# Kernel optimization log

Hardware: AMD Instinct MI355X
Metric: run time of the kernel (lower is better)

Reference implementation:

```python
import jax, jax.numpy as jnp
import numpy as np

C = 256

def setup_inputs() -> dict:
    key = jax.random.key(0)
    ks = jax.random.split(key, 9)
    B, H, W = 32, 32, 32
    s = C ** -0.5  # init scale for weights
    inputs = jax.random.normal(ks[0], (B, H, W, C), jnp.float32)
    Wq = jax.random.normal(ks[1], (C, C), jnp.float32) * s
    Wk = jax.random.normal(ks[2], (C, C), jnp.float32) * s
    Wv = jax.random.normal(ks[3], (C, C), jnp.float32) * s
    Wo = jax.random.normal(ks[4], (C, C), jnp.float32) * s
    bq = jnp.zeros((C,), jnp.float32)
    bk = jnp.zeros((C,), jnp.float32)
    bv = jnp.zeros((C,), jnp.float32)
    bo = jnp.zeros((C,), jnp.float32)
    return {"inputs": inputs, "Wq": Wq, "bq": bq, "Wk": Wk, "bk": bk,
            "Wv": Wv, "bv": bv, "Wo": Wo, "bo": bo}

def reference(inputs, Wq, bq, Wk, bk, Wv, bv, Wo, bo):
    B, H, W, c = inputs.shape
    scale = jnp.float32(c) ** -0.5
    x = inputs.reshape(B, H * W, c)           # 1x1 conv == per-pixel matmul
    q = x @ Wq + bq                           # [B, HW, C]
    k = x @ Wk + bk
    v = x @ Wv + bv
    scores = jnp.einsum('bnc,bmc->bnm', q, k) * scale  # [B, HW, HW]
    attn = jax.nn.softmax(scores, axis=-1)
    attended = jnp.einsum('bnm,bmc->bnc', attn, v)     # [B, HW, C]
    out = attended @ Wo + bo
    return out.reshape(B, H, W, c)
```

## Files before the change

kernel.cpp:

```cpp
#include <hip/hip_runtime.h>
#include <hip/hip_bf16.h>

typedef __bf16 bf16;
typedef __bf16 bf16x8 __attribute__((ext_vector_type(8)));
typedef float f32x4 __attribute__((ext_vector_type(4)));

#define SM_C 0.09016994374947424f

__global__ __launch_bounds__(256) void transpose_w(
    const float* __restrict__ Wq, const float* __restrict__ Wk,
    const float* __restrict__ Wv, const float* __restrict__ Wo,
    bf16* __restrict__ Wt)
{
    int idx = blockIdx.x * 256 + threadIdx.x;
    int m = idx >> 16, r = idx & 65535;
    int n = r >> 8, k = r & 255;
    const float* W = (m == 0) ? Wq : (m == 1) ? Wk : (m == 2) ? Wv : Wo;
    Wt[(size_t)m * 65536 + n * 256 + k] = (bf16)W[k * 256 + n];
}

__global__ __launch_bounds__(256) void qkv_gemm(
    const float* __restrict__ X, const bf16* __restrict__ Wt,
    const float* __restrict__ bq, const float* __restrict__ bk,
    const float* __restrict__ bv,
    bf16* __restrict__ Qo, bf16* __restrict__ Ko, bf16* __restrict__ Vto)
{
    __shared__ bf16 Xs[128 * 264];
    __shared__ bf16 Ws[2][64 * 264];

    const int t    = threadIdx.x;
    const int lane = t & 63, wv = t >> 6;
    const int quad = lane >> 4, l16 = lane & 15;
    const int bm   = blockIdx.x;

    const int m0 = t >> 3;
    const int c0 = (t & 7) * 8;

#pragma unroll
    for (int p = 0; p < 4; ++p) {
#pragma unroll
        for (int kt = 0; kt < 4; ++kt) {
            const float* px = X + (size_t)(bm * 128 + m0 + p * 32) * 256 + kt * 64 + c0;
            f32x4 a = *(const f32x4*)px, b = *(const f32x4*)(px + 4);
            bf16x8 r;
#pragma unroll
            for (int j = 0; j < 4; ++j) { r[j] = (bf16)a[j]; r[j + 4] = (bf16)b[j]; }
            *(bf16x8*)(Xs + (m0 + p * 32) * 264 + kt * 64 + c0) = r;
        }
    }

    const int w0 = t >> 2;
    const int wc = (t & 3) * 8;

    bf16x8 wreg[8];
#pragma unroll
    for (int c = 0; c < 8; ++c)
        wreg[c] = *(const bf16x8*)(Wt + (size_t)w0 * 256 + c * 32 + wc);
#pragma unroll
    for (int c = 0; c < 8; ++c)
        *(bf16x8*)(Ws[0] + w0 * 264 + c * 32 + wc) = wreg[c];
#pragma unroll
    for (int c = 0; c < 8; ++c)
        wreg[c] = *(const bf16x8*)(Wt + (size_t)16384 + w0 * 256 + c * 32 + wc);

    for (int o = 0; o < 12; ++o) {
        __syncthreads();

        if (o < 11) {
#pragma unroll
            for (int c = 0; c < 8; ++c)
                *(bf16x8*)(Ws[(o + 1) & 1] + w0 * 264 + c * 32 + wc) = wreg[c];
            if (o < 10) {
#pragma unroll
                for (int c = 0; c < 8; ++c)
                    wreg[c] = *(const bf16x8*)(Wt + (size_t)(o + 2) * 16384 + w0 * 256 + c * 32 + wc);
            }
        }

        const bf16* Wb = Ws[o & 1];
        const f32x4 zero = {0.0f, 0.0f, 0.0f, 0.0f};
        f32x4 acc[2][4];
        for (int i = 0; i < 2; ++i)
            for (int j = 0; j < 4; ++j) acc[i][j] = zero;

#pragma unroll
        for (int ks = 0; ks < 8; ++ks) {
            bf16x8 a[2], bb[4];
#pragma unroll
            for (int mt = 0; mt < 2; ++mt)
                a[mt] = *(const bf16x8*)(Xs + (wv * 32 + mt * 16 + l16) * 264 + ks * 32 + quad * 8);
#pragma unroll
            for (int nt = 0; nt < 4; ++nt)
                bb[nt] = *(const bf16x8*)(Wb + (nt * 16 + l16) * 264 + ks * 32 + quad * 8);
#pragma unroll
            for (int mt = 0; mt < 2; ++mt)
#pragma unroll
                for (int nt = 0; nt < 4; ++nt)
                    acc[mt][nt] = __builtin_amdgcn_mfma_f32_16x16x32_bf16(
                        a[mt], bb[nt], acc[mt][nt], 0, 0, 0);
        }

        const int proj = o >> 2, nt4 = o & 3;
        const float* bias = (proj == 0) ? bq : (proj == 1) ? bk : bv;
#pragma unroll
        for (int nt = 0; nt < 4; ++nt) {
            int col = nt4 * 64 + nt * 16 + l16;
            float bvv = bias[col];
#pragma unroll
            for (int mt = 0; mt < 2; ++mt) {
#pragma unroll
                for (int r = 0; r < 4; ++r) {
                    int grow = bm * 128 + wv * 32 + mt * 16 + quad * 4 + r;
                    float v = acc[mt][nt][r] + bvv;
                    if (proj == 0) {
                        Qo[(size_t)grow * 256 + col] = (bf16)v;
                    } else if (proj == 1) {
                        Ko[(size_t)grow * 256 + col] = (bf16)v;
                    } else {
                        int b = grow >> 10, m = grow & 1023;
                        Vto[(size_t)b * 262144 + (size_t)col * 1024 + m] = (bf16)v;
                    }
                }
            }
        }
    }
}

__global__ __launch_bounds__(256, 1) void flash_attn(
    const bf16* __restrict__ Qr, const bf16* __restrict__ K,
    const bf16* __restrict__ Vt, bf16* __restrict__ A)
{
    __shared__ bf16 Ks[2][32 * 264];
    __shared__ bf16 Vs[2][256 * 40];
    __shared__ bf16 Ps[4][32 * 32];

    const int t    = threadIdx.x;
    const int lane = t & 63, wv = t >> 6;
    const int quad = lane >> 4, l16 = lane & 15;
    const int b  = blockIdx.x;
    const int qt = blockIdx.y;

    bf16x8 qf[2][8];
#pragma unroll
    for (int mt = 0; mt < 2; ++mt) {
        const size_t qrow = (size_t)b * 1024 + qt * 128 + wv * 32 + mt * 16 + l16;
#pragma unroll
        for (int ks = 0; ks < 8; ++ks)
            qf[mt][ks] = *(const bf16x8*)(Qr + qrow * 256 + ks * 32 + quad * 8);
    }

    const f32x4 zero = {0.0f, 0.0f, 0.0f, 0.0f};
    f32x4 o[2][16];
    for (int mt = 0; mt < 2; ++mt)
        for (int n = 0; n < 16; ++n) o[mt][n] = zero;
    float lst[2][4] = {{0.f, 0.f, 0.f, 0.f}, {0.f, 0.f, 0.f, 0.f}};

    char* Pb = (char*)(Ps[wv]);

    const int kv0 = t >> 5, kc0 = (t & 31) * 8;
    const int vc0 = t >> 2, vm0 = (t & 3) * 8;

    bf16x8 kp[4], vp[4];
#pragma unroll
    for (int p = 0; p < 4; ++p) {
        kp[p] = *(const bf16x8*)(K + (size_t)(b * 1024 + kv0 + p * 8) * 256 + kc0);
        vp[p] = *(const bf16x8*)(Vt + (size_t)b * 262144 + (size_t)(vc0 + p * 64) * 1024 + vm0);
    }
#pragma unroll
    for (int p = 0; p < 4; ++p) {
        *(bf16x8*)(Ks[0] + (kv0 + p * 8) * 264 + kc0) = kp[p];
        *(bf16x8*)(Vs[0] + (vc0 + p * 64) * 40 + vm0) = vp[p];
    }
#pragma unroll
    for (int p = 0; p < 4; ++p) {
        kp[p] = *(const bf16x8*)(K + (size_t)(b * 1024 + 32 + kv0 + p * 8) * 256 + kc0);
        vp[p] = *(const bf16x8*)(Vt + (size_t)b * 262144 + (size_t)(vc0 + p * 64) * 1024 + 32 + vm0);
    }

    for (int j = 0; j < 32; ++j) {
        const bf16* Kb = Ks[j & 1];
        const bf16* Vb = Vs[j & 1];
        __syncthreads();

        f32x4 s[2][2];
        s[0][0] = zero; s[0][1] = zero; s[1][0] = zero; s[1][1] = zero;
#pragma unroll
        for (int ks = 0; ks < 8; ++ks) {
#pragma unroll
            for (int n = 0; n < 2; ++n) {
                bf16x8 bfr = *(const bf16x8*)(Kb + (n * 16 + l16) * 264 + ks * 32 + quad * 8);
                s[0][n] = __builtin_amdgcn_mfma_f32_16x16x32_bf16(qf[0][ks], bfr, s[0][n], 0, 0, 0);
                s[1][n] = __builtin_amdgcn_mfma_f32_16x16x32_bf16(qf[1][ks], bfr, s[1][n], 0, 0, 0);
            }
        }

        if (j < 31) {
            bf16* Kn = Ks[(j + 1) & 1];
            bf16* Vn = Vs[(j + 1) & 1];
#pragma unroll
            for (int p = 0; p < 4; ++p) {
                *(bf16x8*)(Kn + (kv0 + p * 8) * 264 + kc0) = kp[p];
                *(bf16x8*)(Vn + (vc0 + p * 64) * 40 + vm0) = vp[p];
            }
            if (j < 30) {
#pragma unroll
                for (int p = 0; p < 4; ++p) {
                    kp[p] = *(const bf16x8*)(K + (size_t)(b * 1024 + (j + 2) * 32 + kv0 + p * 8) * 256 + kc0);
                    vp[p] = *(const bf16x8*)(Vt + (size_t)b * 262144 + (size_t)(vc0 + p * 64) * 1024 + (j + 2) * 32 + vm0);
                }
            }
        }

#pragma unroll
        for (int mt = 0; mt < 2; ++mt) {
#pragma unroll
            for (int n = 0; n < 2; ++n) {
#pragma unroll
                for (int r = 0; r < 4; ++r) {
                    float pv = __builtin_amdgcn_exp2f(s[mt][n][r] * SM_C);
                    lst[mt][r] += pv;
                    int row = mt * 16 + quad * 4 + r;
                    *(bf16*)(Pb + ((row * 64 + n * 32 + l16 * 2) ^ ((row & 7) << 4))) = (bf16)pv;
                }
            }
        }

        bf16x8 af0 = *(const bf16x8*)(Pb + ((l16 * 64 + quad * 16) ^ ((l16 & 7) << 4)));
        bf16x8 af1 = *(const bf16x8*)(Pb + (((16 + l16) * 64 + quad * 16) ^ ((l16 & 7) << 4)));
#pragma unroll
        for (int n = 0; n < 16; ++n) {
            bf16x8 bfr = *(const bf16x8*)(Vb + (n * 16 + l16) * 40 + quad * 8);
            o[0][n] = __builtin_amdgcn_mfma_f32_16x16x32_bf16(af0, bfr, o[0][n], 0, 0, 0);
            o[1][n] = __builtin_amdgcn_mfma_f32_16x16x32_bf16(af1, bfr, o[1][n], 0, 0, 0);
        }
    }

#pragma unroll
    for (int mt = 0; mt < 2; ++mt) {
#pragma unroll
        for (int r = 0; r < 4; ++r) {
            float l = lst[mt][r];
            for (int off = 1; off < 16; off <<= 1)
                l += __shfl_xor(l, off, 64);
            float inv = 1.0f / l;
            size_t grow = (size_t)b * 1024 + qt * 128 + wv * 32 + mt * 16 + quad * 4 + r;
#pragma unroll
            for (int n = 0; n < 16; ++n)
                A[grow * 256 + n * 16 + l16] = (bf16)(o[mt][n][r] * inv);
        }
    }
}

__global__ __launch_bounds__(256) void oproj_gemm(
    const bf16* __restrict__ Xv, const bf16* __restrict__ W,
    const float* __restrict__ bias, float* __restrict__ outv)
{
    __shared__ bf16 Xs[128 * 72];
    __shared__ bf16 Ws[64 * 72];

    const int t    = threadIdx.x;
    const int lane = t & 63, wv = t >> 6;
    const int quad = lane >> 4, l16 = lane & 15;
    const int bm = blockIdx.x;
    const int bn = blockIdx.y;

    const f32x4 zero = {0.0f, 0.0f, 0.0f, 0.0f};
    f32x4 acc[2][4];
    for (int i = 0; i < 2; ++i)
        for (int j = 0; j < 4; ++j) acc[i][j] = zero;

    const int m0 = t >> 3;
    const int c0 = (t & 7) * 8;

    bf16x8 xp[4], wp[2];
#pragma unroll
    for (int p = 0; p < 4; ++p)
        xp[p] = *(const bf16x8*)(Xv + (size_t)(bm * 128 + m0 + p * 32) * 256 + c0);
#pragma unroll
    for (int p = 0; p < 2; ++p)
        wp[p] = *(const bf16x8*)(W + (size_t)(bn * 64 + m0 + p * 32) * 256 + c0);

    for (int kt = 0; kt < 4; ++kt) {
#pragma unroll
        for (int p = 0; p < 4; ++p)
            *(bf16x8*)(Xs + (m0 + p * 32) * 72 + c0) = xp[p];
#pragma unroll
        for (int p = 0; p < 2; ++p)
            *(bf16x8*)(Ws + (m0 + p * 32) * 72 + c0) = wp[p];
        __syncthreads();

        if (kt < 3) {
#pragma unroll
            for (int p = 0; p < 4; ++p)
                xp[p] = *(const bf16x8*)(Xv + (size_t)(bm * 128 + m0 + p * 32) * 256 + (kt + 1) * 64 + c0);
#pragma unroll
            for (int p = 0; p < 2; ++p)
                wp[p] = *(const bf16x8*)(W + (size_t)(bn * 64 + m0 + p * 32) * 256 + (kt + 1) * 64 + c0);
        }

#pragma unroll
        for (int ks = 0; ks < 2; ++ks) {
            bf16x8 a[2], bb[4];
            for (int mt = 0; mt < 2; ++mt)
                a[mt] = *(const bf16x8*)(Xs + (wv * 32 + mt * 16 + l16) * 72 + ks * 32 + quad * 8);
            for (int nt = 0; nt < 4; ++nt)
                bb[nt] = *(const bf16x8*)(Ws + (nt * 16 + l16) * 72 + ks * 32 + quad * 8);
            for (int mt = 0; mt < 2; ++mt)
                for (int nt = 0; nt < 4; ++nt)
                    acc[mt][nt] = __builtin_amdgcn_mfma_f32_16x16x32_bf16(
                        a[mt], bb[nt], acc[mt][nt], 0, 0, 0);
        }
        __syncthreads();
    }

#pragma unroll
    for (int nt = 0; nt < 4; ++nt) {
        int col = bn * 64 + nt * 16 + l16;
        float bvv = bias[col];
#pragma unroll
        for (int mt = 0; mt < 2; ++mt)
#pragma unroll
            for (int r = 0; r < 4; ++r) {
                int grow = bm * 128 + wv * 32 + mt * 16 + quad * 4 + r;
                outv[(size_t)grow * 256 + col] = acc[mt][nt][r] + bvv;
            }
    }
}

extern "C" void kernel_launch(void* const* d_in, const int* in_sizes, int n_in,
                              void* d_out, int out_size, void* d_ws, size_t ws_size,
                              hipStream_t stream)
{
    (void)in_sizes; (void)n_in; (void)out_size; (void)ws_size;
    const float* X  = (const float*)d_in[0];
    const float* Wq = (const float*)d_in[1];
    const float* bq = (const float*)d_in[2];
    const float* Wk = (const float*)d_in[3];
    const float* bk = (const float*)d_in[4];
    const float* Wv = (const float*)d_in[5];
    const float* bv = (const float*)d_in[6];
    const float* Wo = (const float*)d_in[7];
    const float* bo = (const float*)d_in[8];
    float* out = (float*)d_out;

    const size_t NTOK = (size_t)32768 * 256;

    bf16* Wt  = (bf16*)d_ws;
    bf16* Qw  = (bf16*)d_ws + 262144;
    bf16* Kw  = Qw + NTOK;
    bf16* Vtw = Kw + NTOK;

    transpose_w<<<1024, 256, 0, stream>>>(Wq, Wk, Wv, Wo, Wt);
    qkv_gemm   <<<256,  256, 0, stream>>>(X, Wt, bq, bk, bv, Qw, Kw, Vtw);
    flash_attn <<<dim3(32, 8),  256, 0, stream>>>(Qw, Kw, Vtw, Qw);
    oproj_gemm <<<dim3(256, 4), 256, 0, stream>>>(Qw, Wt + 3 * 65536, bo, out);
}
```

Baseline: 198.7 us.

## Double waves per block in QKV GEMM and flash attention kernels

Both the QKV projection and flash attention kernels go from 256 to 512 threads per block. Each wave now owns 16 query/token rows instead of 32, and the cooperative load indexing is remapped for 512 threads. The grid stays at 256 blocks, so the aim is more waves per CU to hide latency and better use of the MFMA units, with lower register pressure per wave. The cost is that each wave reuses every shared-memory K/V and weight fragment for half as many rows, so LDS read traffic per FLOP doubles.

```diff
diff --git a/kernel.cpp b/kernel.cpp
--- a/kernel.cpp
+++ b/kernel.cpp
@@ -19,7 +19,7 @@
     Wt[(size_t)m * 65536 + n * 256 + k] = (bf16)W[k * 256 + n];
 }
 
-__global__ __launch_bounds__(256) void qkv_gemm(
+__global__ __launch_bounds__(512, 2) void qkv_gemm(
     const float* __restrict__ X, const bf16* __restrict__ Wt,
     const float* __restrict__ bq, const float* __restrict__ bk,
     const float* __restrict__ bv,
@@ -33,71 +33,66 @@
     const int quad = lane >> 4, l16 = lane & 15;
     const int bm   = blockIdx.x;
 
-    const int m0 = t >> 3;
-    const int c0 = (t & 7) * 8;
-
-#pragma unroll
-    for (int p = 0; p < 4; ++p) {
-#pragma unroll
-        for (int kt = 0; kt < 4; ++kt) {
-            const float* px = X + (size_t)(bm * 128 + m0 + p * 32) * 256 + kt * 64 + c0;
-            f32x4 a = *(const f32x4*)px, b = *(const f32x4*)(px + 4);
-            bf16x8 r;
-#pragma unroll
-            for (int j = 0; j < 4; ++j) { r[j] = (bf16)a[j]; r[j + 4] = (bf16)b[j]; }
-            *(bf16x8*)(Xs + (m0 + p * 32) * 264 + kt * 64 + c0) = r;
-        }
-    }
-
-    const int w0 = t >> 2;
-    const int wc = (t & 3) * 8;
-
-    bf16x8 wreg[8];
-#pragma unroll
-    for (int c = 0; c < 8; ++c)
-        wreg[c] = *(const bf16x8*)(Wt + (size_t)w0 * 256 + c * 32 + wc);
-#pragma unroll
-    for (int c = 0; c < 8; ++c)
-        *(bf16x8*)(Ws[0] + w0 * 264 + c * 32 + wc) = wreg[c];
-#pragma unroll
-    for (int c = 0; c < 8; ++c)
-        wreg[c] = *(const bf16x8*)(Wt + (size_t)16384 + w0 * 256 + c * 32 + wc);
+#pragma unroll
+    for (int i = 0; i < 8; ++i) {
+        int c = t + i * 512;
+        int row = c >> 5, cf = (c & 31) * 8;
+        const float* px = X + (size_t)(bm * 128 + row) * 256 + cf;
+        f32x4 a = *(const f32x4*)px, b = *(const f32x4*)(px + 4);
+        bf16x8 r;
+#pragma unroll
+        for (int j = 0; j < 4; ++j) { r[j] = (bf16)a[j]; r[j + 4] = (bf16)b[j]; }
+        *(bf16x8*)(Xs + row * 264 + cf) = r;
+    }
+
+    bf16x8 wreg[4];
+#pragma unroll
+    for (int i = 0; i < 4; ++i) {
+        int c = t + i * 512;
+        wreg[i] = *(const bf16x8*)(Wt + (size_t)(c >> 5) * 256 + (c & 31) * 8);
+    }
+#pragma unroll
+    for (int i = 0; i < 4; ++i) {
+        int c = t + i * 512;
+        *(bf16x8*)(Ws[0] + (c >> 5) * 264 + (c & 31) * 8) = wreg[i];
+    }
+#pragma unroll
+    for (int i = 0; i < 4; ++i) {
+        int c = t + i * 512;
+        wreg[i] = *(const bf16x8*)(Wt + (size_t)16384 + (c >> 5) * 256 + (c & 31) * 8);
+    }
 
     for (int o = 0; o < 12; ++o) {
         __syncthreads();
 
         if (o < 11) {
 #pragma unroll
-            for (int c = 0; c < 8; ++c)
-                *(bf16x8*)(Ws[(o + 1) & 1] + w0 * 264 + c * 32 + wc) = wreg[c];
+            for (int i = 0; i < 4; ++i) {
+                int c = t + i * 512;
+                *(bf16x8*)(Ws[(o + 1) & 1] + (c >> 5) * 264 + (c & 31) * 8) = wreg[i];
+            }
             if (o < 10) {
 #pragma unroll
-                for (int c = 0; c < 8; ++c)
-                    wreg[c] = *(const bf16x8*)(Wt + (size_t)(o + 2) * 16384 + w0 * 256 + c * 32 + wc);
+                for (int i = 0; i < 4; ++i) {
+                    int c = t + i * 512;
+                    wreg[i] = *(const bf16x8*)(Wt + (size_t)(o + 2) * 16384 + (c >> 5) * 256 + (c & 31) * 8);
+                }
             }
         }
 
         const bf16* Wb = Ws[o & 1];
         const f32x4 zero = {0.0f, 0.0f, 0.0f, 0.0f};
-        f32x4 acc[2][4];
-        for (int i = 0; i < 2; ++i)
-            for (int j = 0; j < 4; ++j) acc[i][j] = zero;
+        f32x4 acc[4];
+        acc[0] = zero; acc[1] = zero; acc[2] = zero; acc[3] = zero;
 
 #pragma unroll
         for (int ks = 0; ks < 8; ++ks) {
-            bf16x8 a[2], bb[4];
-#pragma unroll
-            for (int mt = 0; mt < 2; ++mt)
-                a[mt] = *(const bf16x8*)(Xs + (wv * 32 + mt * 16 + l16) * 264 + ks * 32 + quad * 8);
-#pragma unroll
-            for (int nt = 0; nt < 4; ++nt)
-                bb[nt] = *(const bf16x8*)(Wb + (nt * 16 + l16) * 264 + ks * 32 + quad * 8);
-#pragma unroll
-            for (int mt = 0; mt < 2; ++mt)
-#pragma unroll
-                for (int nt = 0; nt < 4; ++nt)
-                    acc[mt][nt] = __builtin_amdgcn_mfma_f32_16x16x32_bf16(
-                        a[mt], bb[nt], acc[mt][nt], 0, 0, 0);
+            bf16x8 a = *(const bf16x8*)(Xs + (wv * 16 + l16) * 264 + ks * 32 + quad * 8);
+#pragma unroll
+            for (int nt = 0; nt < 4; ++nt) {
+                bf16x8 bb = *(const bf16x8*)(Wb + (nt * 16 + l16) * 264 + ks * 32 + quad * 8);
+                acc[nt] = __builtin_amdgcn_mfma_f32_16x16x32_bf16(a, bb, acc[nt], 0, 0, 0);
+            }
         }
 
         const int proj = o >> 2, nt4 = o & 3;
@@ -107,32 +102,29 @@
             int col = nt4 * 64 + nt * 16 + l16;
             float bvv = bias[col];
 #pragma unroll
-            for (int mt = 0; mt < 2; ++mt) {
-#pragma unroll
-                for (int r = 0; r < 4; ++r) {
-                    int grow = bm * 128 + wv * 32 + mt * 16 + quad * 4 + r;
-                    float v = acc[mt][nt][r] + bvv;
-                    if (proj == 0) {
-                        Qo[(size_t)grow * 256 + col] = (bf16)v;
-                    } else if (proj == 1) {
-                        Ko[(size_t)grow * 256 + col] = (bf16)v;
-                    } else {
-                        int b = grow >> 10, m = grow & 1023;
-                        Vto[(size_t)b * 262144 + (size_t)col * 1024 + m] = (bf16)v;
-                    }
+            for (int r = 0; r < 4; ++r) {
+                int grow = bm * 128 + wv * 16 + quad * 4 + r;
+                float v = acc[nt][r] + bvv;
+                if (proj == 0) {
+                    Qo[(size_t)grow * 256 + col] = (bf16)v;
+                } else if (proj == 1) {
+                    Ko[(size_t)grow * 256 + col] = (bf16)v;
+                } else {
+                    int b = grow >> 10, m = grow & 1023;
+                    Vto[(size_t)b * 262144 + (size_t)col * 1024 + m] = (bf16)v;
                 }
             }
         }
     }
 }
 
-__global__ __launch_bounds__(256, 1) void flash_attn(
+__global__ __launch_bounds__(512, 2) void flash_attn(
     const bf16* __restrict__ Qr, const bf16* __restrict__ K,
     const bf16* __restrict__ Vt, bf16* __restrict__ A)
 {
     __shared__ bf16 Ks[2][32 * 264];
     __shared__ bf16 Vs[2][256 * 40];
-    __shared__ bf16 Ps[4][32 * 32];
+    __shared__ bf16 Ps[8][16 * 32];
 
     const int t    = threadIdx.x;
     const int lane = t & 63, wv = t >> 6;
@@ -140,41 +132,38 @@
     const int b  = blockIdx.x;
     const int qt = blockIdx.y;
 
-    bf16x8 qf[2][8];
-#pragma unroll
-    for (int mt = 0; mt < 2; ++mt) {
-        const size_t qrow = (size_t)b * 1024 + qt * 128 + wv * 32 + mt * 16 + l16;
-#pragma unroll
-        for (int ks = 0; ks < 8; ++ks)
-            qf[mt][ks] = *(const bf16x8*)(Qr + qrow * 256 + ks * 32 + quad * 8);
-    }
+    bf16x8 qf[8];
+    const size_t qrow = (size_t)b * 1024 + qt * 128 + wv * 16 + l16;
+#pragma unroll
+    for (int ks = 0; ks < 8; ++ks)
+        qf[ks] = *(const bf16x8*)(Qr + qrow * 256 + ks * 32 + quad * 8);
 
     const f32x4 zero = {0.0f, 0.0f, 0.0f, 0.0f};
-    f32x4 o[2][16];
-    for (int mt = 0; mt < 2; ++mt)
-        for (int n = 0; n < 16; ++n) o[mt][n] = zero;
-    float lst[2][4] = {{0.f, 0.f, 0.f, 0.f}, {0.f, 0.f, 0.f, 0.f}};
+    f32x4 o[16];
+#pragma unroll
+    for (int n = 0; n < 16; ++n) o[n] = zero;
+    float lst[4] = {0.f, 0.f, 0.f, 0.f};
 
     char* Pb = (char*)(Ps[wv]);
 
-    const int kv0 = t >> 5, kc0 = (t & 31) * 8;
-    const int vc0 = t >> 2, vm0 = (t & 3) * 8;
-
-    bf16x8 kp[4], vp[4];
-#pragma unroll
-    for (int p = 0; p < 4; ++p) {
-        kp[p] = *(const bf16x8*)(K + (size_t)(b * 1024 + kv0 + p * 8) * 256 + kc0);
-        vp[p] = *(const bf16x8*)(Vt + (size_t)b * 262144 + (size_t)(vc0 + p * 64) * 1024 + vm0);
-    }
-#pragma unroll
-    for (int p = 0; p < 4; ++p) {
-        *(bf16x8*)(Ks[0] + (kv0 + p * 8) * 264 + kc0) = kp[p];
-        *(bf16x8*)(Vs[0] + (vc0 + p * 64) * 40 + vm0) = vp[p];
-    }
-#pragma unroll
-    for (int p = 0; p < 4; ++p) {
-        kp[p] = *(const bf16x8*)(K + (size_t)(b * 1024 + 32 + kv0 + p * 8) * 256 + kc0);
-        vp[p] = *(const bf16x8*)(Vt + (size_t)b * 262144 + (size_t)(vc0 + p * 64) * 1024 + 32 + vm0);
+    const int kv0 = t >> 4, kc0 = (t & 15) * 8;
+    const int vc0 = t >> 1, vm0 = (t & 1) * 8;
+
+    bf16x8 kp[2], vp[2];
+#pragma unroll
+    for (int p = 0; p < 2; ++p) {
+        kp[p] = *(const bf16x8*)(K + (size_t)(b * 1024 + kv0) * 256 + kc0 + p * 128);
+        vp[p] = *(const bf16x8*)(Vt + (size_t)b * 262144 + (size_t)vc0 * 1024 + vm0 + p * 16);
+    }
+#pragma unroll
+    for (int p = 0; p < 2; ++p) {
+        *(bf16x8*)(Ks[0] + kv0 * 264 + kc0 + p * 128) = kp[p];
+        *(bf16x8*)(Vs[0] + vc0 * 40 + vm0 + p * 16) = vp[p];
+    }
+#pragma unroll
+    for (int p = 0; p < 2; ++p) {
+        kp[p] = *(const bf16x8*)(K + (size_t)(b * 1024 + 32 + kv0) * 256 + kc0 + p * 128);
+        vp[p] = *(const bf16x8*)(Vt + (size_t)b * 262144 + (size_t)vc0 * 1024 + 32 + vm0 + p * 16);
     }
 
     for (int j = 0; j < 32; ++j) {
@@ -182,15 +171,14 @@
         const bf16* Vb = Vs[j & 1];
         __syncthreads();
 
-        f32x4 s[2][2];
-        s[0][0] = zero; s[0][1] = zero; s[1][0] = zero; s[1][1] = zero;
+        f32x4 s[2];
+        s[0] = zero; s[1] = zero;
 #pragma unroll
         for (int ks = 0; ks < 8; ++ks) {
 #pragma unroll
             for (int n = 0; n < 2; ++n) {
                 bf16x8 bfr = *(const bf16x8*)(Kb + (n * 16 + l16) * 264 + ks * 32 + quad * 8);
-                s[0][n] = __builtin_amdgcn_mfma_f32_16x16x32_bf16(qf[0][ks], bfr, s[0][n], 0, 0, 0);
-                s[1][n] = __builtin_amdgcn_mfma_f32_16x16x32_bf16(qf[1][ks], bfr, s[1][n], 0, 0, 0);
+                s[n] = __builtin_amdgcn_mfma_f32_16x16x32_bf16(qf[ks], bfr, s[n], 0, 0, 0);
             }
         }
 
@@ -198,56 +186,48 @@
             bf16* Kn = Ks[(j + 1) & 1];
             bf16* Vn = Vs[(j + 1) & 1];
 #pragma unroll
-            for (int p = 0; p < 4; ++p) {
-                *(bf16x8*)(Kn + (kv0 + p * 8) * 264 + kc0) = kp[p];
-                *(bf16x8*)(Vn + (vc0 + p * 64) * 40 + vm0) = vp[p];
+            for (int p = 0; p < 2; ++p) {
+                *(bf16x8*)(Kn + kv0 * 264 + kc0 + p * 128) = kp[p];
+                *(bf16x8*)(Vn + vc0 * 40 + vm0 + p * 16) = vp[p];
             }
             if (j < 30) {
 #pragma unroll
-                for (int p = 0; p < 4; ++p) {
-                    kp[p] = *(const bf16x8*)(K + (size_t)(b * 1024 + (j + 2) * 32 + kv0 + p * 8) * 256 + kc0);
-                    vp[p] = *(const bf16x8*)(Vt + (size_t)b * 262144 + (size_t)(vc0 + p * 64) * 1024 + (j + 2) * 32 + vm0);
+                for (int p = 0; p < 2; ++p) {
+                    kp[p] = *(const bf16x8*)(K + (size_t)(b * 1024 + (j + 2) * 32 + kv0) * 256 + kc0 + p * 128);
+                    vp[p] = *(const bf16x8*)(Vt + (size_t)b * 262144 + (size_t)vc0 * 1024 + (j + 2) * 32 + vm0 + p * 16);
                 }
             }
         }
 
 #pragma unroll
-        for (int mt = 0; mt < 2; ++mt) {
-#pragma unroll
-            for (int n = 0; n < 2; ++n) {
-#pragma unroll
-                for (int r = 0; r < 4; ++r) {
-                    float pv = __builtin_amdgcn_exp2f(s[mt][n][r] * SM_C);
-                    lst[mt][r] += pv;
-                    int row = mt * 16 + quad * 4 + r;
-                    *(bf16*)(Pb + ((row * 64 + n * 32 + l16 * 2) ^ ((row & 7) << 4))) = (bf16)pv;
-                }
-            }
-        }
-
-        bf16x8 af0 = *(const bf16x8*)(Pb + ((l16 * 64 + quad * 16) ^ ((l16 & 7) << 4)));
-        bf16x8 af1 = *(const bf16x8*)(Pb + (((16 + l16) * 64 + quad * 16) ^ ((l16 & 7) << 4)));
+        for (int n = 0; n < 2; ++n) {
+#pragma unroll
+            for (int r = 0; r < 4; ++r) {
+                float pv = __builtin_amdgcn_exp2f(s[n][r] * SM_C);
+                lst[r] += pv;
+                int row = quad * 4 + r;
+                *(bf16*)(Pb + ((row * 64 + n * 32 + l16 * 2) ^ ((row & 7) << 4))) = (bf16)pv;
+            }
+        }
+
+        bf16x8 af = *(const bf16x8*)(Pb + ((l16 * 64 + quad * 16) ^ ((l16 & 7) << 4)));
 #pragma unroll
         for (int n = 0; n < 16; ++n) {
             bf16x8 bfr = *(const bf16x8*)(Vb + (n * 16 + l16) * 40 + quad * 8);
-            o[0][n] = __builtin_amdgcn_mfma_f32_16x16x32_bf16(af0, bfr, o[0][n], 0, 0, 0);
-            o[1][n] = __builtin_amdgcn_mfma_f32_16x16x32_bf16(af1, bfr, o[1][n], 0, 0, 0);
-        }
-    }
-
-#pragma unroll
-    for (int mt = 0; mt < 2; ++mt) {
-#pragma unroll
-        for (int r = 0; r < 4; ++r) {
-            float l = lst[mt][r];
-            for (int off = 1; off < 16; off <<= 1)
-                l += __shfl_xor(l, off, 64);
-            float inv = 1.0f / l;
-            size_t grow = (size_t)b * 1024 + qt * 128 + wv * 32 + mt * 16 + quad * 4 + r;
-#pragma unroll
-            for (int n = 0; n < 16; ++n)
-                A[grow * 256 + n * 16 + l16] = (bf16)(o[mt][n][r] * inv);
-        }
+            o[n] = __builtin_amdgcn_mfma_f32_16x16x32_bf16(af, bfr, o[n], 0, 0, 0);
+        }
+    }
+
+#pragma unroll
+    for (int r = 0; r < 4; ++r) {
+        float l = lst[r];
+        for (int off = 1; off < 16; off <<= 1)
+            l += __shfl_xor(l, off, 64);
+        float inv = 1.0f / l;
+        size_t grow = (size_t)b * 1024 + qt * 128 + wv * 16 + quad * 4 + r;
+#pragma unroll
+        for (int n = 0; n < 16; ++n)
+            A[grow * 256 + n * 16 + l16] = (bf16)(o[n][r] * inv);
     }
 }
 
@@ -351,7 +331,7 @@
     bf16* Vtw = Kw + NTOK;
 
     transpose_w<<<1024, 256, 0, stream>>>(Wq, Wk, Wv, Wo, Wt);
-    qkv_gemm   <<<256,  256, 0, stream>>>(X, Wt, bq, bk, bv, Qw, Kw, Vtw);
-    flash_attn <<<dim3(32, 8),  256, 0, stream>>>(Qw, Kw, Vtw, Qw);
+    qkv_gemm   <<<256,  512, 0, stream>>>(X, Wt, bq, bk, bv, Qw, Kw, Vtw);
+    flash_attn <<<dim3(32, 8),  512, 0, stream>>>(Qw, Kw, Vtw, Qw);
     oproj_gemm <<<dim3(256, 4), 256, 0, stream>>>(Qw, Wt + 3 * 65536, bo, out);
 }
```

Measured after the change: 187.0 us. 5.9% less time.
